# Kernel optimization log

Measured on AMD Instinct MI355X. Metric: run time of the kernel, lower is better.

The kernel has to match this reference:

```python
import jax, jax.numpy as jnp
import numpy as np

M, K, V, A = 50, 50, 200, 64  # memory_size, key_dim, value_dim, attention_dim
B, S = 512, 1024


def setup_inputs() -> dict:
    key = jax.random.key(0)
    ks = jax.random.split(key, 12)
    kaiming = lambda k, shape, fan_in: jax.random.normal(k, shape, jnp.float32) * np.sqrt(2.0 / fan_in)
    return {
        "query_embeddings": jax.random.normal(ks[0], (B, S, K), jnp.float32),
        "attention_features": jax.random.normal(ks[1], (B, S, A), jnp.float32),
        "value_memory": jax.random.normal(ks[2], (B, M, V), jnp.float32),
        "key_memory": kaiming(ks[3], (M, K), K),
        "Wc": kaiming(ks[4], (K, K), K),   # correlation_projection
        "bc": jnp.zeros((K,), jnp.float32),
        "Wr": kaiming(ks[5], (A, V), V),   # guided_read_projection
        "br": jnp.zeros((A,), jnp.float32),
        "We": kaiming(ks[6], (V, 2 * A), 2 * A),  # erase_gate
        "be": jnp.zeros((V,), jnp.float32),
        "Wa": kaiming(ks[7], (V, 2 * A), 2 * A),  # add_gate
        "ba": jnp.zeros((V,), jnp.float32),
    }


def reference(query_embeddings, attention_features, value_memory,
              key_memory, Wc, bc, Wr, br, We, be, Wa, ba):
    # update_memory=True path: sequential DKVMN read/erase/add over time.

    def read(mem, q_t, a_t):
        ck = jnp.tanh(q_t @ Wc.T + bc)                     # [B,K]
        w = jax.nn.softmax(ck @ key_memory.T, axis=-1)     # [B,M]
        rc = jnp.einsum('bm,bmv->bv', w, mem) @ Wr.T + br  # [B,A]
        return w, rc

    def write(mem, w, a_t, rc):
        wi = jnp.concatenate([a_t, rc], axis=-1)           # [B,2A]
        erase = jax.nn.sigmoid(wi @ We.T + be)             # [B,V]
        add = jnp.tanh(wi @ Wa.T + ba)                     # [B,V]
        w3 = w[:, :, None]
        return mem * (1.0 - w3 * erase[:, None, :]) + w3 * add[:, None, :]

    def step(mem, xs):
        q_t, a_t = xs
        w, rc = read(mem, q_t, a_t)
        return write(mem, w, a_t, rc), (rc, w)

    # first S-1 steps update memory; last step reads only
    q_seq = jnp.swapaxes(query_embeddings[:, :-1], 0, 1)   # [S-1,B,K]
    a_seq = jnp.swapaxes(attention_features[:, :-1], 0, 1)
    mem_final, (rcs, ws) = jax.lax.scan(step, value_memory, (q_seq, a_seq))
    w_last, rc_last = read(mem_final, query_embeddings[:, -1], attention_features[:, -1])

    read_content = jnp.concatenate([jnp.swapaxes(rcs, 0, 1), rc_last[:, None]], axis=1)  # [B,S,A]
    memory_weights = jnp.concatenate([jnp.swapaxes(ws, 0, 1), w_last[:, None]], axis=1)  # [B,S,M]
    return read_content, mem_final, memory_weights
```

## Files before the change

### kernel.cpp

```cpp
#include <hip/hip_runtime.h>
#include <stdint.h>

#define Md 50
#define Kd 50
#define Vd 200
#define Ad 64
#define Bd 512
#define Sd 1024

__device__ __forceinline__ float fast_tanh(float x) {
    float e = __expf(2.f * x);
    return 1.f - 2.f / (e + 1.f);
}

__device__ __forceinline__ float sigmoidf_(float x) {
    return 1.f / (1.f + __expf(-x));
}

__global__ __launch_bounds__(512, 2)
void agm_kernel(const float* __restrict__ q_in,
                const float* __restrict__ a_in,
                const float* __restrict__ mem_in,
                const float* __restrict__ key_in,
                const float* __restrict__ Wc_in,
                const float* __restrict__ bc_in,
                const float* __restrict__ Wr_in,
                const float* __restrict__ br_in,
                const float* __restrict__ We_in,
                const float* __restrict__ be_in,
                const float* __restrict__ Wa_in,
                const float* __restrict__ ba_in,
                float* __restrict__ rc_out,
                float* __restrict__ mem_out,
                float* __restrict__ w_out)
{
    __shared__ float sWcT[Kd * Kd];
    __shared__ float sKeyT[Kd * Md];
    __shared__ float sbc[Kd], sbr[Ad], sbe[Vd], sba[Vd];
    __shared__ float sq[2][Kd];
    __shared__ __align__(16) float swi[2][128];
    __shared__ float sck[2][64];
    __shared__ float sw[2][64];
    __shared__ float srcv[2][Vd];
    __shared__ float ser[2][Vd], sad[2][Vd];

    const int tid = threadIdx.x;
    const int blk = blockIdx.x;

    const int hb = tid >> 8;
    const int mv = tid & 255;
    const int bidx = blk * 2 + hb;

    for (int idx = tid; idx < Kd * Kd; idx += 512) {
        int i = idx / Kd, k = idx % Kd;
        sWcT[k * Kd + i] = Wc_in[idx];
        sKeyT[k * Md + i] = key_in[idx];
    }
    if (tid < Kd) sbc[tid] = bc_in[tid];
    if (tid < Ad) sbr[tid] = br_in[tid];
    if (tid < Vd) { sbe[tid] = be_in[tid]; sba[tid] = ba_in[tid]; }

    const int a4 = ((tid >> 6) << 3) | (tid & 7);
    const int c4 = (tid & 63) >> 3;
    float WrS[25];
    #pragma unroll
    for (int j = 0; j < 25; ++j)
        WrS[j] = Wr_in[a4 * Vd + c4 * 25 + j];

    const int wv = tid >> 1;
    const int wh = tid & 1;
    float WeC[64], WaC[64];
    if (wv < Vd) {
        const float4* wep = (const float4*)(We_in + wv * 128 + wh * 64);
        const float4* wap = (const float4*)(Wa_in + wv * 128 + wh * 64);
        #pragma unroll
        for (int c = 0; c < 16; ++c) {
            float4 ue = wep[c];
            float4 ua = wap[c];
            WeC[4*c+0] = ue.x; WeC[4*c+1] = ue.y;
            WeC[4*c+2] = ue.z; WeC[4*c+3] = ue.w;
            WaC[4*c+0] = ua.x; WaC[4*c+1] = ua.y;
            WaC[4*c+2] = ua.z; WaC[4*c+3] = ua.w;
        }
    } else {
        #pragma unroll
        for (int j = 0; j < 64; ++j) { WeC[j] = 0.f; WaC[j] = 0.f; }
    }

    float memcol[Md];
    if (mv < Vd) {
        #pragma unroll
        for (int m = 0; m < Md; ++m)
            memcol[m] = mem_in[(size_t)bidx * Md * Vd + m * Vd + mv];
    } else {
        #pragma unroll
        for (int m = 0; m < Md; ++m) memcol[m] = 0.f;
    }

    const bool is_q = (tid < 100);
    const int qhb = tid / 50, qk = tid % 50;
    const bool is_a = (tid >= 256 && tid < 384);
    const int ahb = (tid - 256) >> 6, aj = tid & 63;

    float qreg = 0.f, areg = 0.f;
    if (is_q) qreg = q_in[(size_t)(blk * 2 + qhb) * Sd * Kd + qk];
    if (is_a) areg = a_in[(size_t)(blk * 2 + ahb) * Sd * Ad + aj];

    for (int t = 0; t < Sd; ++t) {
        if (is_q) sq[qhb][qk] = qreg;
        if (is_a) swi[ahb][aj] = areg;
        __syncthreads();

        if (t + 1 < Sd) {
            if (is_q) qreg = q_in[(size_t)(blk * 2 + qhb) * Sd * Kd + (t + 1) * Kd + qk];
            if (is_a) areg = a_in[(size_t)(blk * 2 + ahb) * Sd * Ad + (t + 1) * Ad + aj];
        }

        if (mv < Kd) {
            float acc = sbc[mv];
            for (int k = 0; k < Kd; ++k)
                acc = fmaf(sq[hb][k], sWcT[k * Kd + mv], acc);
            sck[hb][mv] = fast_tanh(acc);
        }
        __syncthreads();

        if (mv < 64) {
            int m = mv;
            float lg = -1e30f;
            if (m < Md) {
                lg = 0.f;
                for (int k = 0; k < Kd; ++k)
                    lg = fmaf(sck[hb][k], sKeyT[k * Md + m], lg);
            }
            float mx = lg;
            #pragma unroll
            for (int off = 32; off > 0; off >>= 1)
                mx = fmaxf(mx, __shfl_xor(mx, off));
            float e = (m < Md) ? __expf(lg - mx) : 0.f;
            float sm = e;
            #pragma unroll
            for (int off = 32; off > 0; off >>= 1)
                sm += __shfl_xor(sm, off);
            if (m < Md) sw[hb][m] = e / sm;
        }
        __syncthreads();

        if (mv < Vd) {
            float acc = 0.f;
            #pragma unroll
            for (int m = 0; m < Md; ++m)
                acc = fmaf(sw[hb][m], memcol[m], acc);
            srcv[hb][mv] = acc;
        }
        if (mv < Md) {
            w_out[(size_t)bidx * Sd * Md + (size_t)t * Md + mv] = sw[hb][mv];
        }
        __syncthreads();

        {
            float p0 = 0.f, p1 = 0.f;
            #pragma unroll
            for (int j = 0; j < 25; ++j) {
                int v = c4 * 25 + j;
                p0 = fmaf(srcv[0][v], WrS[j], p0);
                p1 = fmaf(srcv[1][v], WrS[j], p1);
            }
            #pragma unroll
            for (int off = 8; off < 64; off <<= 1) {
                p0 += __shfl_xor(p0, off);
                p1 += __shfl_xor(p1, off);
            }
            if ((tid & 63) < 8) {
                float rc0 = p0 + sbr[a4];
                float rc1 = p1 + sbr[a4];
                swi[0][64 + a4] = rc0;
                swi[1][64 + a4] = rc1;
                rc_out[(size_t)(blk * 2 + 0) * Sd * Ad + (size_t)t * Ad + a4] = rc0;
                rc_out[(size_t)(blk * 2 + 1) * Sd * Ad + (size_t)t * Ad + a4] = rc1;
            }
        }
        __syncthreads();

        if (t < Sd - 1) {
            float pe0 = 0.f, pa0 = 0.f, pe1 = 0.f, pa1 = 0.f;
            {
                const float4* w0p = (const float4*)&swi[0][wh * 64];
                const float4* w1p = (const float4*)&swi[1][wh * 64];
                #pragma unroll
                for (int j4 = 0; j4 < 16; ++j4) {
                    float4 x0 = w0p[j4];
                    float4 x1 = w1p[j4];
                    pe0 = fmaf(x0.x, WeC[4*j4+0], pe0);
                    pe0 = fmaf(x0.y, WeC[4*j4+1], pe0);
                    pe0 = fmaf(x0.z, WeC[4*j4+2], pe0);
                    pe0 = fmaf(x0.w, WeC[4*j4+3], pe0);
                    pa0 = fmaf(x0.x, WaC[4*j4+0], pa0);
                    pa0 = fmaf(x0.y, WaC[4*j4+1], pa0);
                    pa0 = fmaf(x0.z, WaC[4*j4+2], pa0);
                    pa0 = fmaf(x0.w, WaC[4*j4+3], pa0);
                    pe1 = fmaf(x1.x, WeC[4*j4+0], pe1);
                    pe1 = fmaf(x1.y, WeC[4*j4+1], pe1);
                    pe1 = fmaf(x1.z, WeC[4*j4+2], pe1);
                    pe1 = fmaf(x1.w, WeC[4*j4+3], pe1);
                    pa1 = fmaf(x1.x, WaC[4*j4+0], pa1);
                    pa1 = fmaf(x1.y, WaC[4*j4+1], pa1);
                    pa1 = fmaf(x1.z, WaC[4*j4+2], pa1);
                    pa1 = fmaf(x1.w, WaC[4*j4+3], pa1);
                }
            }
            pe0 += __shfl_xor(pe0, 1);
            pa0 += __shfl_xor(pa0, 1);
            pe1 += __shfl_xor(pe1, 1);
            pa1 += __shfl_xor(pa1, 1);
            if (wh == 0 && wv < Vd) {
                ser[0][wv] = sigmoidf_(pe0 + sbe[wv]);
                sad[0][wv] = fast_tanh(pa0 + sba[wv]);
                ser[1][wv] = sigmoidf_(pe1 + sbe[wv]);
                sad[1][wv] = fast_tanh(pa1 + sba[wv]);
            }
            __syncthreads();

            if (mv < Vd) {
                float ev = ser[hb][mv], av = sad[hb][mv];
                #pragma unroll
                for (int m = 0; m < Md; ++m) {
                    float wm = sw[hb][m];
                    float inner = fmaf(-ev, memcol[m], av);
                    memcol[m] = fmaf(wm, inner, memcol[m]);
                }
            }
        }
    }

    if (mv < Vd) {
        #pragma unroll
        for (int m = 0; m < Md; ++m)
            mem_out[(size_t)bidx * Md * Vd + m * Vd + mv] = memcol[m];
    }
}

extern "C" void kernel_launch(void* const* d_in, const int* in_sizes, int n_in,
                              void* d_out, int out_size, void* d_ws, size_t ws_size,
                              hipStream_t stream) {
    const float* q   = (const float*)d_in[0];
    const float* a   = (const float*)d_in[1];
    const float* mem = (const float*)d_in[2];
    const float* key = (const float*)d_in[3];
    const float* Wc  = (const float*)d_in[4];
    const float* bc  = (const float*)d_in[5];
    const float* Wr  = (const float*)d_in[6];
    const float* br  = (const float*)d_in[7];
    const float* We  = (const float*)d_in[8];
    const float* be  = (const float*)d_in[9];
    const float* Wa  = (const float*)d_in[10];
    const float* ba  = (const float*)d_in[11];

    float* out = (float*)d_out;
    float* rc_out  = out;
    float* mem_out = rc_out + (size_t)Bd * Sd * Ad;
    float* w_out   = mem_out + (size_t)Bd * Md * Vd;

    hipLaunchKernelGGL(agm_kernel, dim3(256), dim3(512), 0, stream,
                       q, a, mem, key, Wc, bc, Wr, br, We, be, Wa, ba,
                       rc_out, mem_out, w_out);
}
```

Measured before the change: 6.342 ms.

## Software-pipeline recurrence: overlap next-step softmax with gate dots, cut barriers

Restructures the per-timestep loop so that the query-key softmax for step t+1 runs on idle waves while other waves compute the attention-half gate dot products. The gate dot products are split across waves and reduce through shared memory, and the Wr projection is moved into transposed shared memory. Broadcasts of per-step vectors now use readlane instead of shared-memory loads. The aim is fewer __syncthreads per step and a shorter serial dependency chain. The cost is more shared memory, double-buffered state and more complex index logic.

```diff
diff --git a/kernel.cpp b/kernel.cpp
--- a/kernel.cpp
+++ b/kernel.cpp
@@ -15,6 +15,10 @@
 
 __device__ __forceinline__ float sigmoidf_(float x) {
     return 1.f / (1.f + __expf(-x));
+}
+
+__device__ __forceinline__ float rl(float v, int l) {
+    return __uint_as_float((unsigned)__builtin_amdgcn_readlane((int)__float_as_uint(v), l));
 }
 
 __global__ __launch_bounds__(512, 2)
@@ -36,56 +40,55 @@
 {
     __shared__ float sWcT[Kd * Kd];
     __shared__ float sKeyT[Kd * Md];
+    __shared__ __align__(16) float sWrT[Vd * 66];
     __shared__ float sbc[Kd], sbr[Ad], sbe[Vd], sba[Vd];
-    __shared__ float sq[2][Kd];
+    __shared__ float sq[2][2][Kd];
+    __shared__ float sw[2][2][64];
     __shared__ __align__(16) float swi[2][128];
-    __shared__ float sck[2][64];
-    __shared__ float sw[2][64];
-    __shared__ float srcv[2][Vd];
-    __shared__ float ser[2][Vd], sad[2][Vd];
+    __shared__ __align__(16) float srcvI[Vd * 2];
+    __shared__ float spe[2][2][Vd];
+    __shared__ float spa[2][2][Vd];
 
     const int tid = threadIdx.x;
     const int blk = blockIdx.x;
-
-    const int hb = tid >> 8;
-    const int mv = tid & 255;
+    const int hb  = tid >> 8;
+    const int mv  = tid & 255;
+    const int wv  = tid >> 6;
+    const int ln  = tid & 63;
     const int bidx = blk * 2 + hb;
 
     for (int idx = tid; idx < Kd * Kd; idx += 512) {
         int i = idx / Kd, k = idx % Kd;
-        sWcT[k * Kd + i] = Wc_in[idx];
+        sWcT[k * Kd + i]  = Wc_in[idx];
         sKeyT[k * Md + i] = key_in[idx];
+    }
+    for (int idx = tid; idx < Ad * Vd; idx += 512) {
+        int a = idx / Vd, v = idx % Vd;
+        sWrT[v * 66 + a] = Wr_in[idx];
     }
     if (tid < Kd) sbc[tid] = bc_in[tid];
     if (tid < Ad) sbr[tid] = br_in[tid];
     if (tid < Vd) { sbe[tid] = be_in[tid]; sba[tid] = ba_in[tid]; }
 
-    const int a4 = ((tid >> 6) << 3) | (tid & 7);
-    const int c4 = (tid & 63) >> 3;
-    float WrS[25];
-    #pragma unroll
-    for (int j = 0; j < 25; ++j)
-        WrS[j] = Wr_in[a4 * Vd + c4 * 25 + j];
-
-    const int wv = tid >> 1;
-    const int wh = tid & 1;
+    const int wh5 = wv >> 2;
+    const int r5  = (wv & 3) * 50 + ln;
     float WeC[64], WaC[64];
-    if (wv < Vd) {
-        const float4* wep = (const float4*)(We_in + wv * 128 + wh * 64);
-        const float4* wap = (const float4*)(Wa_in + wv * 128 + wh * 64);
+    if (ln < 50) {
+        const float4* wep = (const float4*)(We_in + (size_t)r5 * 128 + wh5 * 64);
+        const float4* wap = (const float4*)(Wa_in + (size_t)r5 * 128 + wh5 * 64);
         #pragma unroll
         for (int c = 0; c < 16; ++c) {
-            float4 ue = wep[c];
-            float4 ua = wap[c];
-            WeC[4*c+0] = ue.x; WeC[4*c+1] = ue.y;
-            WeC[4*c+2] = ue.z; WeC[4*c+3] = ue.w;
-            WaC[4*c+0] = ua.x; WaC[4*c+1] = ua.y;
-            WaC[4*c+2] = ua.z; WaC[4*c+3] = ua.w;
+            float4 ue = wep[c], ua = wap[c];
+            WeC[4*c+0]=ue.x; WeC[4*c+1]=ue.y; WeC[4*c+2]=ue.z; WeC[4*c+3]=ue.w;
+            WaC[4*c+0]=ua.x; WaC[4*c+1]=ua.y; WaC[4*c+2]=ua.z; WaC[4*c+3]=ua.w;
         }
     } else {
         #pragma unroll
         for (int j = 0; j < 64; ++j) { WeC[j] = 0.f; WaC[j] = 0.f; }
     }
+
+    const int g4 = (tid >> 3) & 31;
+    const int c4 = tid & 7;
 
     float memcol[Md];
     if (mv < Vd) {
@@ -102,134 +105,156 @@
     const bool is_a = (tid >= 256 && tid < 384);
     const int ahb = (tid - 256) >> 6, aj = tid & 63;
 
+    auto fused_s1s2 = [&](int par, int h) {
+        float ckv = 0.f;
+        if (ln < Kd) {
+            float acc = sbc[ln];
+            #pragma unroll
+            for (int k = 0; k < Kd; ++k)
+                acc = fmaf(sq[par][h][k], sWcT[k * Kd + ln], acc);
+            ckv = fast_tanh(acc);
+        }
+        float lg = -1e30f;
+        if (ln < Md) {
+            float l0 = 0.f, l1 = 0.f;
+            #pragma unroll
+            for (int k = 0; k < Kd; k += 2) {
+                l0 = fmaf(rl(ckv, k),     sKeyT[k * Md + ln],       l0);
+                l1 = fmaf(rl(ckv, k + 1), sKeyT[(k + 1) * Md + ln], l1);
+            }
+            lg = l0 + l1;
+        }
+        float mx = lg;
+        #pragma unroll
+        for (int off = 32; off > 0; off >>= 1)
+            mx = fmaxf(mx, __shfl_xor(mx, off));
+        float e = (ln < Md) ? __expf(lg - mx) : 0.f;
+        float sm = e;
+        #pragma unroll
+        for (int off = 32; off > 0; off >>= 1)
+            sm += __shfl_xor(sm, off);
+        if (ln < Md) sw[par][h][ln] = e / sm;
+    };
+
+    auto s5dot = [&](int xoff, int whi) {
+        float xA = swi[0][xoff + ln];
+        float xB = swi[1][xoff + ln];
+        float pe0 = 0.f, pa0 = 0.f, pe1 = 0.f, pa1 = 0.f;
+        #pragma unroll
+        for (int j = 0; j < 64; ++j) {
+            float sa = rl(xA, j);
+            float sb = rl(xB, j);
+            pe0 = fmaf(sa, WeC[j], pe0);
+            pa0 = fmaf(sa, WaC[j], pa0);
+            pe1 = fmaf(sb, WeC[j], pe1);
+            pa1 = fmaf(sb, WaC[j], pa1);
+        }
+        if (ln < 50) {
+            spe[whi][0][r5] = pe0; spe[whi][1][r5] = pe1;
+            spa[whi][0][r5] = pa0; spa[whi][1][r5] = pa1;
+        }
+    };
+
+    if (is_q) {
+        sq[0][qhb][qk] = q_in[(size_t)(blk*2+qhb) * Sd * Kd + qk];
+        sq[1][qhb][qk] = q_in[(size_t)(blk*2+qhb) * Sd * Kd + Kd + qk];
+    }
+    if (is_a) swi[ahb][aj] = a_in[(size_t)(blk*2+ahb) * Sd * Ad + aj];
+    __syncthreads();
+
+    if (wv == 2 || wv == 3) fused_s1s2(0, wv - 2);
+
     float qreg = 0.f, areg = 0.f;
-    if (is_q) qreg = q_in[(size_t)(blk * 2 + qhb) * Sd * Kd + qk];
-    if (is_a) areg = a_in[(size_t)(blk * 2 + ahb) * Sd * Ad + aj];
+    if (is_q) qreg = q_in[(size_t)(blk*2+qhb) * Sd * Kd + 2 * Kd + qk];
+    if (is_a) areg = a_in[(size_t)(blk*2+ahb) * Sd * Ad + Ad + aj];
+    __syncthreads();
+
+    float swreg = sw[0][hb][ln];
+    if (mv < Vd) {
+        float p0 = 0.f, p1 = 0.f;
+        #pragma unroll
+        for (int m = 0; m < Md; m += 2) {
+            p0 = fmaf(rl(swreg, m),     memcol[m],     p0);
+            p1 = fmaf(rl(swreg, m + 1), memcol[m + 1], p1);
+        }
+        srcvI[mv * 2 + hb] = p0 + p1;
+    }
+    if (mv < Md) w_out[(size_t)bidx * Sd * Md + mv] = swreg;
 
     for (int t = 0; t < Sd; ++t) {
-        if (is_q) sq[qhb][qk] = qreg;
-        if (is_a) swi[ahb][aj] = areg;
         __syncthreads();
 
-        if (t + 1 < Sd) {
-            if (is_q) qreg = q_in[(size_t)(blk * 2 + qhb) * Sd * Kd + (t + 1) * Kd + qk];
-            if (is_a) areg = a_in[(size_t)(blk * 2 + ahb) * Sd * Ad + (t + 1) * Ad + aj];
-        }
-
-        if (mv < Kd) {
-            float acc = sbc[mv];
-            for (int k = 0; k < Kd; ++k)
-                acc = fmaf(sq[hb][k], sWcT[k * Kd + mv], acc);
-            sck[hb][mv] = fast_tanh(acc);
-        }
-        __syncthreads();
-
-        if (mv < 64) {
-            int m = mv;
-            float lg = -1e30f;
-            if (m < Md) {
-                lg = 0.f;
-                for (int k = 0; k < Kd; ++k)
-                    lg = fmaf(sck[hb][k], sKeyT[k * Md + m], lg);
-            }
-            float mx = lg;
-            #pragma unroll
-            for (int off = 32; off > 0; off >>= 1)
-                mx = fmaxf(mx, __shfl_xor(mx, off));
-            float e = (m < Md) ? __expf(lg - mx) : 0.f;
-            float sm = e;
-            #pragma unroll
-            for (int off = 32; off > 0; off >>= 1)
-                sm += __shfl_xor(sm, off);
-            if (m < Md) sw[hb][m] = e / sm;
-        }
-        __syncthreads();
-
-        if (mv < Vd) {
-            float acc = 0.f;
-            #pragma unroll
-            for (int m = 0; m < Md; ++m)
-                acc = fmaf(sw[hb][m], memcol[m], acc);
-            srcv[hb][mv] = acc;
-        }
-        if (mv < Md) {
-            w_out[(size_t)bidx * Sd * Md + (size_t)t * Md + mv] = sw[hb][mv];
-        }
-        __syncthreads();
-
-        {
-            float p0 = 0.f, p1 = 0.f;
+        if (wv >= 4) {
+            float q00 = 0.f, q01 = 0.f, q10 = 0.f, q11 = 0.f;
             #pragma unroll
             for (int j = 0; j < 25; ++j) {
                 int v = c4 * 25 + j;
-                p0 = fmaf(srcv[0][v], WrS[j], p0);
-                p1 = fmaf(srcv[1][v], WrS[j], p1);
-            }
-            #pragma unroll
-            for (int off = 8; off < 64; off <<= 1) {
-                p0 += __shfl_xor(p0, off);
-                p1 += __shfl_xor(p1, off);
-            }
-            if ((tid & 63) < 8) {
-                float rc0 = p0 + sbr[a4];
-                float rc1 = p1 + sbr[a4];
-                swi[0][64 + a4] = rc0;
-                swi[1][64 + a4] = rc1;
-                rc_out[(size_t)(blk * 2 + 0) * Sd * Ad + (size_t)t * Ad + a4] = rc0;
-                rc_out[(size_t)(blk * 2 + 1) * Sd * Ad + (size_t)t * Ad + a4] = rc1;
-            }
+                float2 sv = *(const float2*)&srcvI[v * 2];
+                float2 wr = *(const float2*)&sWrT[v * 66 + 2 * g4];
+                q00 = fmaf(sv.x, wr.x, q00);
+                q01 = fmaf(sv.y, wr.x, q01);
+                q10 = fmaf(sv.x, wr.y, q10);
+                q11 = fmaf(sv.y, wr.y, q11);
+            }
+            #pragma unroll
+            for (int off = 1; off < 8; off <<= 1) {
+                q00 += __shfl_xor(q00, off);
+                q01 += __shfl_xor(q01, off);
+                q10 += __shfl_xor(q10, off);
+                q11 += __shfl_xor(q11, off);
+            }
+            if (c4 == 0) {
+                int a0 = 2 * g4, a1 = a0 + 1;
+                float rc00 = q00 + sbr[a0], rc01 = q01 + sbr[a0];
+                float rc10 = q10 + sbr[a1], rc11 = q11 + sbr[a1];
+                swi[0][64 + a0] = rc00; swi[1][64 + a0] = rc01;
+                swi[0][64 + a1] = rc10; swi[1][64 + a1] = rc11;
+                size_t o0 = (size_t)(blk*2+0) * Sd * Ad + (size_t)t * Ad;
+                size_t o1 = (size_t)(blk*2+1) * Sd * Ad + (size_t)t * Ad;
+                rc_out[o0 + a0] = rc00; rc_out[o1 + a0] = rc01;
+                rc_out[o0 + a1] = rc10; rc_out[o1 + a1] = rc11;
+            }
+        } else if (t < Sd - 1) {
+            s5dot(0, 0);
         }
         __syncthreads();
 
-        if (t < Sd - 1) {
-            float pe0 = 0.f, pa0 = 0.f, pe1 = 0.f, pa1 = 0.f;
-            {
-                const float4* w0p = (const float4*)&swi[0][wh * 64];
-                const float4* w1p = (const float4*)&swi[1][wh * 64];
-                #pragma unroll
-                for (int j4 = 0; j4 < 16; ++j4) {
-                    float4 x0 = w0p[j4];
-                    float4 x1 = w1p[j4];
-                    pe0 = fmaf(x0.x, WeC[4*j4+0], pe0);
-                    pe0 = fmaf(x0.y, WeC[4*j4+1], pe0);
-                    pe0 = fmaf(x0.z, WeC[4*j4+2], pe0);
-                    pe0 = fmaf(x0.w, WeC[4*j4+3], pe0);
-                    pa0 = fmaf(x0.x, WaC[4*j4+0], pa0);
-                    pa0 = fmaf(x0.y, WaC[4*j4+1], pa0);
-                    pa0 = fmaf(x0.z, WaC[4*j4+2], pa0);
-                    pa0 = fmaf(x0.w, WaC[4*j4+3], pa0);
-                    pe1 = fmaf(x1.x, WeC[4*j4+0], pe1);
-                    pe1 = fmaf(x1.y, WeC[4*j4+1], pe1);
-                    pe1 = fmaf(x1.z, WeC[4*j4+2], pe1);
-                    pe1 = fmaf(x1.w, WeC[4*j4+3], pe1);
-                    pa1 = fmaf(x1.x, WaC[4*j4+0], pa1);
-                    pa1 = fmaf(x1.y, WaC[4*j4+1], pa1);
-                    pa1 = fmaf(x1.z, WaC[4*j4+2], pa1);
-                    pa1 = fmaf(x1.w, WaC[4*j4+3], pa1);
-                }
-            }
-            pe0 += __shfl_xor(pe0, 1);
-            pa0 += __shfl_xor(pa0, 1);
-            pe1 += __shfl_xor(pe1, 1);
-            pa1 += __shfl_xor(pa1, 1);
-            if (wh == 0 && wv < Vd) {
-                ser[0][wv] = sigmoidf_(pe0 + sbe[wv]);
-                sad[0][wv] = fast_tanh(pa0 + sba[wv]);
-                ser[1][wv] = sigmoidf_(pe1 + sbe[wv]);
-                sad[1][wv] = fast_tanh(pa1 + sba[wv]);
-            }
-            __syncthreads();
-
-            if (mv < Vd) {
-                float ev = ser[hb][mv], av = sad[hb][mv];
-                #pragma unroll
-                for (int m = 0; m < Md; ++m) {
-                    float wm = sw[hb][m];
-                    float inner = fmaf(-ev, memcol[m], av);
-                    memcol[m] = fmaf(wm, inner, memcol[m]);
-                }
-            }
-        }
+        if (t == Sd - 1) break;
+
+        if (wv >= 4) {
+            s5dot(64, 1);
+        } else if (wv >= 2) {
+            fused_s1s2((t + 1) & 1, wv - 2);
+        }
+        __syncthreads();
+
+        if (mv < Vd) {
+            float ev = sigmoidf_(spe[0][hb][mv] + spe[1][hb][mv] + sbe[mv]);
+            float av = fast_tanh(spa[0][hb][mv] + spa[1][hb][mv] + sba[mv]);
+            #pragma unroll
+            for (int m = 0; m < Md; ++m) {
+                float wm = rl(swreg, m);
+                memcol[m] = fmaf(wm, fmaf(-ev, memcol[m], av), memcol[m]);
+            }
+        }
+        if (is_a) swi[ahb][aj] = areg;
+        if (is_q && t + 2 < Sd) sq[(t + 2) & 1][qhb][qk] = qreg;
+        if (is_a && t + 2 < Sd)
+            areg = a_in[(size_t)(blk*2+ahb) * Sd * Ad + (size_t)(t + 2) * Ad + aj];
+        if (is_q && t + 3 < Sd)
+            qreg = q_in[(size_t)(blk*2+qhb) * Sd * Kd + (size_t)(t + 3) * Kd + qk];
+        swreg = sw[(t + 1) & 1][hb][ln];
+        if (mv < Vd) {
+            float p0 = 0.f, p1 = 0.f;
+            #pragma unroll
+            for (int m = 0; m < Md; m += 2) {
+                p0 = fmaf(rl(swreg, m),     memcol[m],     p0);
+                p1 = fmaf(rl(swreg, m + 1), memcol[m + 1], p1);
+            }
+            srcvI[mv * 2 + hb] = p0 + p1;
+        }
+        if (mv < Md)
+            w_out[(size_t)bidx * Sd * Md + (size_t)(t + 1) * Md + mv] = swreg;
     }
 
     if (mv < Vd) {
```

After: 5.920 ms. 6.6% less time.
